# Kernel tuning notes

Measured on AMD Instinct MI355X. Metric: run time of the kernel, lower is better.

## Reference

```python
import jax, jax.numpy as jnp
import numpy as np

EPS = 1e-5  # torch BatchNorm1d default eps
O, T, D, H1, H2 = 8, 4, 256, 64, 32


def setup_inputs() -> dict:
    key = jax.random.key(0)
    ks = jax.random.split(key, 8)
    B = 65536
    feature = jax.random.normal(ks[0], (B, D), dtype=jnp.float32)
    treatment = jax.random.randint(ks[1], (B,), 0, T, dtype=jnp.int64)
    s1 = 1.0 / np.sqrt(D)
    s2 = 1.0 / np.sqrt(H1)
    s3 = 1.0 / np.sqrt(H2)
    params = {
        # per (outcome, treatment) expert MLP weights
        'W1': jax.random.uniform(ks[2], (O, T, D, H1), jnp.float32, -s1, s1),
        'b1': jnp.zeros((O, T, H1), jnp.float32),
        'g1': jnp.ones((O, T, H1), jnp.float32),   # BN1 gamma
        'be1': jnp.zeros((O, T, H1), jnp.float32),  # BN1 beta
        'm1': jnp.zeros((O, T, H1), jnp.float32),   # BN1 running mean
        'v1': jnp.ones((O, T, H1), jnp.float32),    # BN1 running var
        'W2': jax.random.uniform(ks[3], (O, T, H1, H2), jnp.float32, -s2, s2),
        'b2': jnp.zeros((O, T, H2), jnp.float32),
        'g2': jnp.ones((O, T, H2), jnp.float32),
        'be2': jnp.zeros((O, T, H2), jnp.float32),
        'm2': jnp.zeros((O, T, H2), jnp.float32),
        'v2': jnp.ones((O, T, H2), jnp.float32),
        'W3': jax.random.uniform(ks[4], (O, T, H2), jnp.float32, -s3, s3),  # final Linear(32,1), squeezed
        'b3': jnp.zeros((O, T), jnp.float32),
    }
    return {'feature': feature, 'treatment': treatment, **params}


def _tlearner_fwd(x, t, W1, b1, g1, be1, m1, v1, W2, b2, g2, be2, m2, v2, W3, b3):
    # Dense evaluation of every (outcome, treatment) expert, then per-row
    # selection by treatment id. Equivalent (in eval mode: BN uses running
    # stats, dropout off) to the masked dispatch of the original module.
    h = jnp.einsum('bd,otdh->both', x, W1) + b1          # [B,O,T,H1]
    h = jax.nn.relu(h)
    h = (h - m1) * jax.lax.rsqrt(v1 + EPS) * g1 + be1    # BN1 (eval)
    h = jnp.einsum('both,othk->botk', h, W2) + b2        # [B,O,T,H2]
    h = jax.nn.relu(h)
    h = (h - m2) * jax.lax.rsqrt(v2 + EPS) * g2 + be2    # BN2 (eval)
    out = jnp.einsum('botk,otk->bot', h, W3) + b3        # [B,O,T]
    idx = t.astype(jnp.int32)[:, None, None]             # [B,1,1]
    return jnp.take_along_axis(out, jnp.broadcast_to(idx, (out.shape[0], O, 1)), axis=2)[..., 0]  # [B,O]


def reference(feature, treatment, W1, b1, g1, be1, m1, v1, W2, b2, g2, be2, m2, v2, W3, b3):
    return _tlearner_fwd(feature, treatment, W1, b1, g1, be1, m1, v1,
                         W2, b2, g2, be2, m2, v2, W3, b3)
```

## Files before the change

kernel.cpp:

```cpp
#include <hip/hip_runtime.h>
#include <cstdint>

typedef short bf16x8 __attribute__((ext_vector_type(8)));
typedef float f32x4 __attribute__((ext_vector_type(4)));

#define NO 8
#define NT 4
#define ND 256
#define NH1 64
#define NH2 32
#define BM 32
#define BNEPS 1e-5f

__device__ __forceinline__ unsigned bfpack2(float a, float b) {
    unsigned ua = __float_as_uint(a), ub = __float_as_uint(b);
    ua = (ua + 0x7FFFu + ((ua >> 16) & 1u)) >> 16;
    ub = (ub + 0x7FFFu + ((ub >> 16) & 1u)) >> 16;
    return ua | (ub << 16);
}


__global__ void k_hist_prep(const int* __restrict__ trt, int* __restrict__ ws, int B,
                            const float* __restrict__ W1, const float* __restrict__ W2,
                            const float* __restrict__ b1, const float* __restrict__ g1,
                            const float* __restrict__ be1, const float* __restrict__ m1,
                            const float* __restrict__ v1,
                            const float* __restrict__ b2, const float* __restrict__ g2,
                            const float* __restrict__ be2, const float* __restrict__ m2,
                            const float* __restrict__ v2, const float* __restrict__ W3,
                            unsigned* __restrict__ W1T4, unsigned* __restrict__ W2T4,
                            float* __restrict__ P1, float* __restrict__ P2) {
    const int bid = blockIdx.x, tid = threadIdx.x;
    if (bid < 256) {
        __shared__ int loc[NT];
        if (tid < NT) loc[tid] = 0;
        __syncthreads();
        const int i = bid * 256 + tid;
        if (i < B) atomicAdd(&loc[trt[i] & 3], 1);
        __syncthreads();
        if (tid < NT) atomicAdd(&ws[tid], loc[tid]);
    } else if (bid < 512) {
        const int gi = (bid - 256) * 256 + tid;
        const int lane = gi & 63, nt = (gi >> 6) & 31, c = (gi >> 11) & 7, t = gi >> 14;
        const int n16 = lane & 15, kg = lane >> 4;
        const int n = nt * 16 + n16, o = n >> 6, h = n & 63;
        const int k0 = c * 32 + kg * 8;
        const float* src = W1 + ((size_t)(o * NT + t) * ND + k0) * NH1 + h;
        float v[8];
#pragma unroll
        for (int j = 0; j < 8; ++j) v[j] = src[(size_t)j * NH1];
        uint4 q;
        q.x = bfpack2(v[0], v[1]); q.y = bfpack2(v[2], v[3]);
        q.z = bfpack2(v[4], v[5]); q.w = bfpack2(v[6], v[7]);
        ((uint4*)W1T4)[gi] = q;
    } else if (bid < 544) {
        const int gi = (bid - 512) * 256 + tid;
        const int m16 = gi & 15, kg = (gi >> 4) & 3, ks = (gi >> 6) & 1,
                  kt = (gi >> 7) & 1, o = (gi >> 8) & 7, t = gi >> 11;
        const int k2 = kt * 16 + m16, hb = ks * 32 + kg * 8;
        const float* src = W2 + ((size_t)(o * NT + t) * NH1 + hb) * NH2 + k2;
        float v[8];
#pragma unroll
        for (int j = 0; j < 8; ++j) v[j] = src[(size_t)j * NH2];
        uint4 q;
        q.x = bfpack2(v[0], v[1]); q.y = bfpack2(v[2], v[3]);
        q.z = bfpack2(v[4], v[5]); q.w = bfpack2(v[6], v[7]);
        ((uint4*)W2T4)[gi] = q;
    } else if (bid < 552) {
        const int gi = (bid - 544) * 256 + tid;
        const int t = gi >> 9, n = gi & 511;
        const int o = n >> 6, h = n & 63;
        const int idx = (o * NT + t) * NH1 + h;
        const float sc = g1[idx] * rsqrtf(v1[idx] + BNEPS);
        P1[gi] = sc;
        P1[2048 + gi] = be1[idx] - m1[idx] * sc;
        P1[4096 + gi] = b1[idx];
    } else {
        const int gi = (bid - 552) * 256 + tid;
        const int t = gi >> 8, q = gi & 255;
        const int o = q >> 5, k2 = q & 31;
        const int idx = (o * NT + t) * NH2 + k2;
        const float s = g2[idx] * rsqrtf(v2[idx] + BNEPS);
        const float w3 = W3[idx];
        P2[gi] = s * w3;
        P2[1024 + gi] = (be2[idx] - m2[idx] * s) * w3;
        P2[2048 + gi] = b2[idx];
    }
}

__global__ void k_scatter(const int* __restrict__ trt, int* __restrict__ ws,
                          int* __restrict__ perm, int B) {
    __shared__ int loc[NT], gb[NT];
    const int tid = threadIdx.x;
    if (tid < NT) loc[tid] = 0;
    __syncthreads();
    const int i = blockIdx.x * blockDim.x + tid;
    int tt = 0, pos = 0;
    if (i < B) { tt = trt[i] & 3; pos = atomicAdd(&loc[tt], 1); }
    __syncthreads();
    if (tid < NT) {
        const int c0 = ws[0], c1 = ws[1], c2 = ws[2];
        const int ub = tid == 0 ? 0 : tid == 1 ? c0 : tid == 2 ? c0 + c1 : c0 + c1 + c2;
        gb[tid] = ub + atomicAdd(&ws[4 + tid], loc[tid]);
    }
    __syncthreads();
    if (i < B) perm[gb[tt] + pos] = i;
}

__global__ __launch_bounds__(256, 3) void k_main(
    const float* __restrict__ X, const int* __restrict__ ws, const int* __restrict__ perm,
    const char* __restrict__ W1T, const char* __restrict__ W2T,
    const float* __restrict__ P1, const float* __restrict__ P2,
    const float* __restrict__ pb3, float* __restrict__ out)
{
    const int c0 = ws[0], c1 = ws[1], c2 = ws[2], c3 = ws[3];
    const int q0 = (c0 + 31) & ~31, q1 = (c1 + 31) & ~31, q2 = (c2 + 31) & ~31;
    const int e0 = q0, e1 = q0 + q1, e2 = e1 + q2, e3 = e2 + ((c3 + 31) & ~31);
    const int m0 = blockIdx.x * BM;
    if (m0 >= e3) return;
    const int t = (m0 >= e0) + (m0 >= e1) + (m0 >= e2);
    const int pb = t == 0 ? 0 : t == 1 ? e0 : t == 2 ? e1 : e2;
    const int ub = t == 0 ? 0 : t == 1 ? c0 : t == 2 ? c0 + c1 : c0 + c1 + c2;
    const int n_t = t == 0 ? c0 : t == 1 ? c1 : t == 2 ? c2 : c3;
    const int ploc0 = m0 - pb;

    const int tid = threadIdx.x;
    const int w = tid >> 6;
    const int l = tid & 63;

    __shared__ __align__(16) char LDS[32768];

    const int pl = ploc0 + (l & 31);
    const int rid_l = perm[ub + min(pl, n_t - 1)];

#pragma unroll
    for (int j = 0; j < 8; ++j) {
        const int r = w * 8 + j;
        const int rr = __shfl(rid_l, r);
        const float4 xv = *(const float4*)(X + (size_t)rr * ND + l * 4);
        uint2 pk;
        pk.x = bfpack2(xv.x, xv.y);
        pk.y = bfpack2(xv.z, xv.w);
        *(uint2*)(LDS + r * 512 + ((l * 8) ^ ((r & 7) << 4))) = pk;
    }

    f32x4 acc[8][2];
#pragma unroll
    for (int nt = 0; nt < 8; ++nt)
#pragma unroll
        for (int rt = 0; rt < 2; ++rt) acc[nt][rt] = (f32x4){0.f, 0.f, 0.f, 0.f};

    const char* W1Tt = W1T + (size_t)t * 262144;
    const char* W1Tw = W1Tt + (w * 8) * 1024 + l * 16;
    const int ln4 = (l >> 4) * 4;

    bf16x8 aA[8], aB[8];
#pragma unroll
    for (int nt = 0; nt < 8; ++nt)
        aA[nt] = *(const bf16x8*)(W1Tw + nt * 1024);

    __syncthreads();

#pragma unroll
    for (int c = 0; c < 8; ++c) {
        if (c < 7) {
            if ((c & 1) == 0) {
#pragma unroll
                for (int nt = 0; nt < 8; ++nt)
                    aB[nt] = *(const bf16x8*)(W1Tw + (c + 1) * 32768 + nt * 1024);
            } else {
#pragma unroll
                for (int nt = 0; nt < 8; ++nt)
                    aA[nt] = *(const bf16x8*)(W1Tw + (c + 1) * 32768 + nt * 1024);
            }
        }
#pragma unroll
        for (int rt = 0; rt < 2; ++rt) {
            const int r = rt * 16 + (l & 15);
            const bf16x8 bX = *(const bf16x8*)(LDS + r * 512 +
                                               ((c * 64 + (l >> 4) * 16) ^ ((r & 7) << 4)));
            if ((c & 1) == 0) {
#pragma unroll
                for (int nt = 0; nt < 8; ++nt)
                    acc[nt][rt] = __builtin_amdgcn_mfma_f32_16x16x32_bf16(aA[nt], bX, acc[nt][rt], 0, 0, 0);
            } else {
#pragma unroll
                for (int nt = 0; nt < 8; ++nt)
                    acc[nt][rt] = __builtin_amdgcn_mfma_f32_16x16x32_bf16(aB[nt], bX, acc[nt][rt], 0, 0, 0);
            }
        }
    }
    __syncthreads();

#pragma unroll
    for (int nt = 0; nt < 8; ++nt) {
        const int n0 = (w * 8 + nt) * 16 + ln4;
        const int p = t * 512 + n0;
        const float4 scv = *(const float4*)(P1 + p);
        const float4 shv = *(const float4*)(P1 + 2048 + p);
        const float4 bbv = *(const float4*)(P1 + 4096 + p);
#pragma unroll
        for (int rt = 0; rt < 2; ++rt) {
            const int r = rt * 16 + (l & 15);
            const f32x4 a = acc[nt][rt];
            const float z0 = fmaf(fmaxf(a[0] + bbv.x, 0.f), scv.x, shv.x);
            const float z1 = fmaf(fmaxf(a[1] + bbv.y, 0.f), scv.y, shv.y);
            const float z2 = fmaf(fmaxf(a[2] + bbv.z, 0.f), scv.z, shv.z);
            const float z3 = fmaf(fmaxf(a[3] + bbv.w, 0.f), scv.w, shv.w);
            uint2 pk;
            pk.x = bfpack2(z0, z1); pk.y = bfpack2(z2, z3);
            *(uint2*)(LDS + r * 1024 + (((unsigned)(n0 * 2)) ^ (unsigned)((r & 7) << 4))) = pk;
        }
    }

    bf16x8 aW[2][2][2];
#pragma unroll
    for (int oo = 0; oo < 2; ++oo) {
        const int o = w * 2 + oo;
#pragma unroll
        for (int kt = 0; kt < 2; ++kt)
#pragma unroll
            for (int ks = 0; ks < 2; ++ks)
                aW[oo][kt][ks] = *(const bf16x8*)(W2T +
                    ((((size_t)t * NO + o) * 2 + kt) * 2 + ks) * 1024 + l * 16);
    }
    f32x4 acc2[2][2][2];
#pragma unroll
    for (int oo = 0; oo < 2; ++oo)
#pragma unroll
        for (int kt = 0; kt < 2; ++kt)
#pragma unroll
            for (int rt2 = 0; rt2 < 2; ++rt2) acc2[oo][kt][rt2] = (f32x4){0.f, 0.f, 0.f, 0.f};

#pragma unroll
    for (int rt2 = 0; rt2 < 2; ++rt2) {
        const int r = rt2 * 16 + (l & 15);
        const unsigned swz = (unsigned)((r & 7) << 4);
#pragma unroll
        for (int ks = 0; ks < 2; ++ks) {
            const int nb = ks * 32 + (l >> 4) * 8;
#pragma unroll
            for (int oo = 0; oo < 2; ++oo) {
                const int n8 = (w * 2 + oo) * 64 + nb;
                const bf16x8 bH = *(const bf16x8*)(LDS + r * 1024 + (((unsigned)(n8 * 2)) ^ swz));
#pragma unroll
                for (int kt = 0; kt < 2; ++kt)
                    acc2[oo][kt][rt2] = __builtin_amdgcn_mfma_f32_16x16x32_bf16(aW[oo][kt][ks], bH, acc2[oo][kt][rt2], 0, 0, 0);
            }
        }
    }

    float p[2][2];
#pragma unroll
    for (int oo = 0; oo < 2; ++oo)
#pragma unroll
        for (int rt2 = 0; rt2 < 2; ++rt2) p[oo][rt2] = 0.f;

#pragma unroll
    for (int oo = 0; oo < 2; ++oo) {
        const int o = w * 2 + oo;
#pragma unroll
        for (int kt = 0; kt < 2; ++kt) {
            const int q = o * 32 + kt * 16 + ln4;
            const int p3 = t * 256 + q;
            const float4 A3 = *(const float4*)(P2 + p3);
            const float4 C3 = *(const float4*)(P2 + 1024 + p3);
            const float4 bb = *(const float4*)(P2 + 2048 + p3);
#pragma unroll
            for (int rt2 = 0; rt2 < 2; ++rt2) {
                const f32x4 a = acc2[oo][kt][rt2];
                float s = fmaf(fmaxf(a[0] + bb.x, 0.f), A3.x, C3.x);
                s = fmaf(fmaxf(a[1] + bb.y, 0.f), A3.y, s + C3.y);
                s = fmaf(fmaxf(a[2] + bb.z, 0.f), A3.z, s + C3.z);
                s = fmaf(fmaxf(a[3] + bb.w, 0.f), A3.w, s + C3.w);
                p[oo][rt2] += s;
            }
        }
    }
#pragma unroll
    for (int oo = 0; oo < 2; ++oo)
#pragma unroll
        for (int rt2 = 0; rt2 < 2; ++rt2) {
            float v = p[oo][rt2];
            v += __shfl_xor(v, 16);
            v += __shfl_xor(v, 32);
            p[oo][rt2] = v;
        }

    const int oo_s = l >> 5;
    const int rt2_s = (l >> 4) & 1;
    const int o_s = w * 2 + oo_s;
    const int r = rt2_s * 16 + (l & 15);
    const float v = oo_s ? (rt2_s ? p[1][1] : p[1][0]) : (rt2_s ? p[0][1] : p[0][0]);
    const int ra = __shfl(rid_l, r);
    if (ploc0 + r < n_t) out[(size_t)ra * NO + o_s] = v + pb3[o_s * NT + t];
}

extern "C" void kernel_launch(void* const* d_in, const int* in_sizes, int n_in,
                              void* d_out, int out_size, void* d_ws, size_t ws_size,
                              hipStream_t stream) {
    const float* X   = (const float*)d_in[0];
    const int* trt   = (const int*)d_in[1];
    const float* W1  = (const float*)d_in[2];
    const float* b1  = (const float*)d_in[3];
    const float* g1  = (const float*)d_in[4];
    const float* be1 = (const float*)d_in[5];
    const float* m1  = (const float*)d_in[6];
    const float* v1  = (const float*)d_in[7];
    const float* W2  = (const float*)d_in[8];
    const float* b2  = (const float*)d_in[9];
    const float* g2  = (const float*)d_in[10];
    const float* be2 = (const float*)d_in[11];
    const float* m2  = (const float*)d_in[12];
    const float* v2  = (const float*)d_in[13];
    const float* W3  = (const float*)d_in[14];
    const float* b3  = (const float*)d_in[15];
    float* out = (float*)d_out;

    const int B = in_sizes[1];
    int* wsi  = (int*)d_ws;
    int* perm = wsi + 16;
    char* wsb = (char*)d_ws;
    size_t off = (64 + (size_t)B * 4 + 15) & ~(size_t)15;
    char* W1T = wsb + off;
    char* W2T = W1T + 1048576;
    float* P1 = (float*)(W2T + 131072);
    float* P2 = P1 + 6144;

    hipMemsetAsync(wsi, 0, 64, stream);
    k_hist_prep<<<556, 256, 0, stream>>>(trt, wsi, B, W1, W2,
                                         b1, g1, be1, m1, v1,
                                         b2, g2, be2, m2, v2, W3,
                                         (unsigned*)W1T, (unsigned*)W2T, P1, P2);
    k_scatter<<<(B + 255) / 256, 256, 0, stream>>>(trt, wsi, perm, B);

    const int gx = (B + 31) / 32 + 4;
    k_main<<<gx, 256, 0, stream>>>(X, wsi, perm, W1T, W2T, P1, P2, b3, out);
}
```

Baseline: 59.47 us.

## Pre-sort and bf16-pack X into padded buffer, load via global_load_lds

After: 77.16 us. 1.3x slower.

```diff
diff --git a/kernel.cpp b/kernel.cpp
--- a/kernel.cpp
+++ b/kernel.cpp
@@ -89,7 +89,7 @@
 }
 
 __global__ void k_scatter(const int* __restrict__ trt, int* __restrict__ ws,
-                          int* __restrict__ perm, int B) {
+                          int* __restrict__ rperm, int* __restrict__ iperm, int B) {
     __shared__ int loc[NT], gb[NT];
     const int tid = threadIdx.x;
     if (tid < NT) loc[tid] = 0;
@@ -100,15 +100,40 @@
     __syncthreads();
     if (tid < NT) {
         const int c0 = ws[0], c1 = ws[1], c2 = ws[2];
-        const int ub = tid == 0 ? 0 : tid == 1 ? c0 : tid == 2 ? c0 + c1 : c0 + c1 + c2;
-        gb[tid] = ub + atomicAdd(&ws[4 + tid], loc[tid]);
-    }
-    __syncthreads();
-    if (i < B) perm[gb[tt] + pos] = i;
+        const int q0 = (c0 + 31) & ~31, q1 = (c1 + 31) & ~31, q2 = (c2 + 31) & ~31;
+        const int eb = tid == 0 ? 0 : tid == 1 ? q0 : tid == 2 ? q0 + q1 : q0 + q1 + q2;
+        gb[tid] = eb + atomicAdd(&ws[4 + tid], loc[tid]);
+    }
+    __syncthreads();
+    if (i < B) {
+        const int p = gb[tt] + pos;
+        rperm[p] = i;
+        iperm[i] = p;
+    }
+}
+
+__global__ __launch_bounds__(256) void k_xcopy(const float* __restrict__ X,
+                                               const int* __restrict__ iperm,
+                                               char* __restrict__ Xs, int B) {
+    const int w = threadIdx.x >> 6, l = threadIdx.x & 63;
+    const int i0 = (blockIdx.x * 4 + w) * 32;
+#pragma unroll 4
+    for (int j = 0; j < 32; ++j) {
+        const int i = i0 + j;
+        if (i < B) {
+            const int s = iperm[i];
+            const float4 xv = *(const float4*)(X + (size_t)i * ND + l * 4);
+            uint2 pk;
+            pk.x = bfpack2(xv.x, xv.y);
+            pk.y = bfpack2(xv.z, xv.w);
+            *(uint2*)(Xs + (size_t)s * 512 + ((l * 8) ^ ((s & 7) << 4))) = pk;
+        }
+    }
 }
 
 __global__ __launch_bounds__(256, 3) void k_main(
-    const float* __restrict__ X, const int* __restrict__ ws, const int* __restrict__ perm,
+    const float* __restrict__ X, const int* __restrict__ ws, const int* __restrict__ rperm,
+    const char* __restrict__ Xs, const int useXs,
     const char* __restrict__ W1T, const char* __restrict__ W2T,
     const float* __restrict__ P1, const float* __restrict__ P2,
     const float* __restrict__ pb3, float* __restrict__ out)
@@ -119,10 +144,6 @@
     const int m0 = blockIdx.x * BM;
     if (m0 >= e3) return;
     const int t = (m0 >= e0) + (m0 >= e1) + (m0 >= e2);
-    const int pb = t == 0 ? 0 : t == 1 ? e0 : t == 2 ? e1 : e2;
-    const int ub = t == 0 ? 0 : t == 1 ? c0 : t == 2 ? c0 + c1 : c0 + c1 + c2;
-    const int n_t = t == 0 ? c0 : t == 1 ? c1 : t == 2 ? c2 : c3;
-    const int ploc0 = m0 - pb;
 
     const int tid = threadIdx.x;
     const int w = tid >> 6;
@@ -130,18 +151,29 @@
 
     __shared__ __align__(16) char LDS[32768];
 
-    const int pl = ploc0 + (l & 31);
-    const int rid_l = perm[ub + min(pl, n_t - 1)];
-
-#pragma unroll
-    for (int j = 0; j < 8; ++j) {
-        const int r = w * 8 + j;
-        const int rr = __shfl(rid_l, r);
-        const float4 xv = *(const float4*)(X + (size_t)rr * ND + l * 4);
-        uint2 pk;
-        pk.x = bfpack2(xv.x, xv.y);
-        pk.y = bfpack2(xv.z, xv.w);
-        *(uint2*)(LDS + r * 512 + ((l * 8) ^ ((r & 7) << 4))) = pk;
+    const int rid_o = rperm[m0 + (l & 31)];
+
+    if (useXs) {
+        const size_t srow = (size_t)(m0 + w * 8) * 512 + (size_t)(l * 16);
+#pragma unroll
+        for (int u = 0; u < 4; ++u) {
+            __builtin_amdgcn_global_load_lds(
+                (const __attribute__((address_space(1))) void*)(Xs + srow + u * 1024),
+                (__attribute__((address_space(3))) void*)(LDS + w * 4096 + l * 16 + u * 1024),
+                16, 0, 0);
+        }
+    } else {
+#pragma unroll
+        for (int j = 0; j < 8; ++j) {
+            const int r = w * 8 + j;
+            const int rr = __shfl(rid_o, r);
+            const int rrow = rr < 0 ? 0 : rr;
+            const float4 xv = *(const float4*)(X + (size_t)rrow * ND + l * 4);
+            uint2 pk;
+            pk.x = bfpack2(xv.x, xv.y);
+            pk.y = bfpack2(xv.z, xv.w);
+            *(uint2*)(LDS + r * 512 + ((l * 8) ^ ((r & 7) << 4))) = pk;
+        }
     }
 
     f32x4 acc[8][2];
@@ -292,8 +324,8 @@
     const int o_s = w * 2 + oo_s;
     const int r = rt2_s * 16 + (l & 15);
     const float v = oo_s ? (rt2_s ? p[1][1] : p[1][0]) : (rt2_s ? p[0][1] : p[0][0]);
-    const int ra = __shfl(rid_l, r);
-    if (ploc0 + r < n_t) out[(size_t)ra * NO + o_s] = v + pb3[o_s * NT + t];
+    const int ra = __shfl(rid_o, r);
+    if (ra >= 0) out[(size_t)ra * NO + o_s] = v + pb3[o_s * NT + t];
 }
 
 extern "C" void kernel_launch(void* const* d_in, const int* in_sizes, int n_in,
@@ -318,22 +350,34 @@
     float* out = (float*)d_out;
 
     const int B = in_sizes[1];
-    int* wsi  = (int*)d_ws;
-    int* perm = wsi + 16;
-    char* wsb = (char*)d_ws;
-    size_t off = (64 + (size_t)B * 4 + 15) & ~(size_t)15;
+    int* wsi   = (int*)d_ws;
+    int* rperm = wsi + 16;
+    int* iperm = rperm + (B + 128);
+    char* wsb  = (char*)d_ws;
+    size_t off = 64 + (size_t)(B + 128) * 4 + (size_t)B * 4;
+    off = (off + 15) & ~(size_t)15;
     char* W1T = wsb + off;
     char* W2T = W1T + 1048576;
     float* P1 = (float*)(W2T + 131072);
     float* P2 = P1 + 6144;
+    size_t endP = off + 1048576 + 131072 + 6144 * 4 + 3072 * 4;
+    size_t offXs = (endP + 511) & ~(size_t)511;
+    char* Xs = wsb + offXs;
+    const size_t need = offXs + (size_t)(B + 128) * 512;
+    const int useXs = (ws_size >= need) ? 1 : 0;
 
     hipMemsetAsync(wsi, 0, 64, stream);
+    hipMemsetAsync(rperm, 0xFF, (size_t)(B + 128) * 4, stream);
+
     k_hist_prep<<<556, 256, 0, stream>>>(trt, wsi, B, W1, W2,
                                          b1, g1, be1, m1, v1,
                                          b2, g2, be2, m2, v2, W3,
                                          (unsigned*)W1T, (unsigned*)W2T, P1, P2);
-    k_scatter<<<(B + 255) / 256, 256, 0, stream>>>(trt, wsi, perm, B);
-
-    const int gx = (B + 31) / 32 + 4;
-    k_main<<<gx, 256, 0, stream>>>(X, wsi, perm, W1T, W2T, P1, P2, b3, out);
-}
+    k_scatter<<<(B + 255) / 256, 256, 0, stream>>>(trt, wsi, rperm, iperm, B);
+    if (useXs)
+        k_xcopy<<<(B + 127) / 128, 256, 0, stream>>>(X, iperm, Xs, B);
+
+    const int gx = (B + 128) / 32;
+    k_main<<<gx, 256, 0, stream>>>(X, wsi, rperm, Xs, useXs,
+                                   W1T, W2T, P1, P2, b3, out);
+}
```
